# Optimization experiments

Hardware: AMD Instinct MI355X
Metric: run time of the kernel (lower is better)

Reference implementation:

```python
import jax, jax.numpy as jnp
import numpy as np

B, S, D = 4, 2048, 1024
H, Dh = 16, 64


def setup_inputs() -> dict:
    key = jax.random.key(0)
    ks = jax.random.split(key, 9)
    s_in = 1.0 / np.sqrt(D)
    inp = {
        "key": jax.random.normal(ks[0], (B, S, D), jnp.float32),
        "value": jax.random.normal(ks[1], (B, S, D), jnp.float32),
        "query": jax.random.normal(ks[2], (B, S, D), jnp.float32),
        # Linear weights stored as [in, out] (math-equivalent to torch W.T)
        "Wq": jax.random.uniform(ks[3], (D, H * Dh), jnp.float32, -s_in, s_in),
        "bq": jax.random.uniform(ks[4], (H * Dh,), jnp.float32, -s_in, s_in),
        "Wk": jax.random.uniform(ks[5], (D, H * Dh), jnp.float32, -s_in, s_in),
        "bk": jax.random.uniform(ks[6], (H * Dh,), jnp.float32, -s_in, s_in),
        "Wv": jax.random.uniform(ks[7], (D, H * Dh), jnp.float32, -s_in, s_in),
        "bv": jax.random.uniform(ks[8], (H * Dh,), jnp.float32, -s_in, s_in),
    }
    return inp


def reference(key, value, query, Wq, bq, Wk, bk, Wv, bv):
    b, s, _ = key.shape
    # projections -> [B, H, S, Dh]
    q = (query @ Wq + bq).reshape(b, s, H, Dh).transpose(0, 2, 1, 3)
    k = (key @ Wk + bk).reshape(b, s, H, Dh).transpose(0, 2, 1, 3)
    v = (value @ Wv + bv).reshape(b, s, H, Dh).transpose(0, 2, 1, 3)
    scores = jnp.einsum("bhqd,bhkd->bhqk", q, k) / np.sqrt(Dh).astype(np.float32)
    p = jax.nn.softmax(scores, axis=-1)
    out = jnp.einsum("bhqk,bhkd->bhqd", p, v)  # [B, H, S, Dh]
    return out.transpose(0, 2, 1, 3).reshape(b, s, H * Dh)
```

## Files before the change

kernel.cpp:

```cpp
#include <hip/hip_runtime.h>

typedef __bf16 bf16;
typedef __bf16 bf16x8 __attribute__((ext_vector_type(8)));
typedef __bf16 bf16x4 __attribute__((ext_vector_type(4)));
typedef _Float16 f16x2 __attribute__((ext_vector_type(2)));
typedef _Float16 f16x4 __attribute__((ext_vector_type(4)));
typedef _Float16 f16x8 __attribute__((ext_vector_type(8)));
typedef __fp16 h16x2 __attribute__((ext_vector_type(2)));
typedef __fp16 h16x4 __attribute__((ext_vector_type(4)));
typedef float  f32x4  __attribute__((ext_vector_type(4)));
typedef float  f32x16 __attribute__((ext_vector_type(16)));

#define LOG2E 1.44269504088896340736f
#define SCQ (0.125f * LOG2E)

__device__ __forceinline__ void async16(const void* g, void* l) {
  __builtin_amdgcn_global_load_lds(
      (const __attribute__((address_space(1))) unsigned int*)g,
      (__attribute__((address_space(3))) unsigned int*)l, 16, 0, 0);
}

__device__ __forceinline__ f32x4 mfma_bf16(bf16x8 a, bf16x8 b, f32x4 c) {
  return __builtin_amdgcn_mfma_f32_16x16x32_bf16(a, b, c, 0, 0, 0);
}
__device__ __forceinline__ f32x16 mfma32_bf16(bf16x8 a, bf16x8 b, f32x16 c) {
  return __builtin_amdgcn_mfma_f32_32x32x16_bf16(a, b, c, 0, 0, 0);
}
__device__ __forceinline__ f32x16 mfma32x8_f16(f16x4 a, f16x4 b, f32x16 c) {
  return __builtin_amdgcn_mfma_f32_32x32x8f16(a, b, c, 0, 0, 0);
}

__global__ __launch_bounds__(256) void prep(const float* __restrict__ q,
                                            const float* __restrict__ k,
                                            const float* __restrict__ v,
                                            const float* __restrict__ W0,
                                            const float* __restrict__ W1,
                                            const float* __restrict__ W2,
                                            bf16* __restrict__ actb,
                                            bf16* __restrict__ Wt) {
  __shared__ float t[64 * 69];
  const int z = blockIdx.y, tid = threadIdx.x;
  if (blockIdx.x < 4096) {
    const float* in = z == 0 ? q : (z == 1 ? k : v);
    bf16* o = actb + (size_t)z * 8388608;
    int i = blockIdx.x * 256 + tid;
    const float4* p = (const float4*)in;
    float4 a = p[i * 2], c = p[i * 2 + 1];
    bf16x8 r;
    r[0] = (bf16)a.x; r[1] = (bf16)a.y; r[2] = (bf16)a.z; r[3] = (bf16)a.w;
    r[4] = (bf16)c.x; r[5] = (bf16)c.y; r[6] = (bf16)c.z; r[7] = (bf16)c.w;
    ((bf16x8*)o)[i] = r;
  } else {
    const float* W = z == 0 ? W0 : (z == 1 ? W1 : W2);
    bf16* O = Wt + (size_t)z * (1024 * 1024);
    int lin = blockIdx.x - 4096;
    int k0 = (lin & 15) * 64, n0 = (lin >> 4) * 64;
    int r0 = tid >> 4, c0 = (tid & 15) * 4;
#pragma unroll
    for (int rr = 0; rr < 4; rr++) {
      int kk = r0 + rr * 16;
      float4 vv = *(const float4*)(W + (k0 + kk) * 1024 + n0 + c0);
      t[kk * 69 + c0 + 0] = vv.x; t[kk * 69 + c0 + 1] = vv.y;
      t[kk * 69 + c0 + 2] = vv.z; t[kk * 69 + c0 + 3] = vv.w;
    }
    __syncthreads();
#pragma unroll
    for (int rr = 0; rr < 4; rr++) {
      int n = r0 + rr * 16;
      bf16x4 o;
#pragma unroll
      for (int j = 0; j < 4; j++) o[j] = (bf16)t[(c0 + j) * 69 + n];
      *(bf16x4*)(O + (n0 + n) * 1024 + k0 + c0) = o;
    }
  }
}

__global__ __launch_bounds__(256, 3) void gemm_qkv(const bf16* __restrict__ Act,
                                                   const bf16* __restrict__ Wt,
                                                   const float* __restrict__ b0,
                                                   const float* __restrict__ b1,
                                                   const float* __restrict__ b2,
                                                   bf16* __restrict__ qo,
                                                   bf16* __restrict__ ko,
                                                   _Float16* __restrict__ vf) {
  __shared__ bf16 smem[16384];
  bf16* sA = smem;
  bf16* sB = smem + 8192;
  const int tid = threadIdx.x;
  const int wave = tid >> 6, lane = tid & 63;
  const int quad = lane >> 4, l15 = lane & 15;
  const int z = blockIdx.z;
  const int m0 = blockIdx.x * 128, n0 = blockIdx.y * 128;
  const bf16* A = Act + (size_t)z * 8388608;
  const bf16* Bt = Wt + (size_t)z * 1048576;
  const float* bias = z == 0 ? b0 : (z == 1 ? b1 : b2);

  const bf16* ap[4]; const bf16* bp[4]; int lo[4];
#pragma unroll
  for (int i = 0; i < 4; i++) {
    int g = wave * 256 + i * 64 + lane;
    int row = g >> 3, jl = (g & 7) ^ (row & 7);
    ap[i] = A + (m0 + row) * 1024 + jl * 8;
    bp[i] = Bt + (n0 + row) * 1024 + jl * 8;
    lo[i] = (wave * 256 + i * 64) * 8;
  }
  const int wm = (wave & 1) * 64, wn = (wave >> 1) * 64;
  f32x4 acc[4][4] = {};

  for (int kt = 0; kt < 16; kt++) {
    const int ko_ = kt * 64;
#pragma unroll
    for (int i = 0; i < 4; i++) async16(ap[i] + ko_, sA + lo[i]);
#pragma unroll
    for (int i = 0; i < 4; i++) async16(bp[i] + ko_, sB + lo[i]);
    __syncthreads();
#pragma unroll
    for (int ks = 0; ks < 2; ks++) {
      bf16x8 af[4], bv[4];
#pragma unroll
      for (int mt = 0; mt < 4; mt++) {
        int m = wm + mt * 16 + l15;
        int ph = (ks * 4 + quad) ^ (m & 7);
        af[mt] = *(const bf16x8*)(sA + m * 64 + ph * 8);
      }
#pragma unroll
      for (int nt = 0; nt < 4; nt++) {
        int n = wn + nt * 16 + l15;
        int ph = (ks * 4 + quad) ^ (n & 7);
        bv[nt] = *(const bf16x8*)(sB + n * 64 + ph * 8);
      }
#pragma unroll
      for (int mt = 0; mt < 4; mt++)
#pragma unroll
        for (int nt = 0; nt < 4; nt++)
          acc[mt][nt] = mfma_bf16(af[mt], bv[nt], acc[mt][nt]);
    }
    __syncthreads();
  }

  if (z != 2) {
    bf16* O = z == 0 ? qo : ko;
    const float sc = z == 0 ? SCQ : 1.0f;
#pragma unroll
    for (int nt = 0; nt < 4; nt++) {
      int n = n0 + wn + nt * 16 + l15;
      float bc = bias[n];
#pragma unroll
      for (int mt = 0; mt < 4; mt++)
#pragma unroll
        for (int r = 0; r < 4; r++) {
          int m = m0 + wm + mt * 16 + quad * 4 + r;
          O[m * 1024 + n] = (bf16)((acc[mt][nt][r] + bc) * sc);
        }
    }
  } else {
    const int b = m0 >> 11, s0 = m0 & 2047;
    const int kvb = s0 >> 7;
    const int mtg0 = (wave & 1) * 4;
    const int w = quad >> 1, hl = quad & 1;
#pragma unroll
    for (int nt = 0; nt < 4; nt++) {
      int n = n0 + wn + nt * 16;
      int hh = n >> 6, db = (n >> 5) & 1;
      int lanep = hl * 32 + (nt & 1) * 16 + l15;
      float bc = bias[n + l15];
#pragma unroll
      for (int mt = 0; mt < 4; mt++) {
        int fi = (mtg0 + mt) * 2 + db;
        f16x4 pk;
#pragma unroll
        for (int r = 0; r < 4; r++) pk[r] = (_Float16)(acc[mt][nt][r] + bc);
        size_t off = ((((size_t)(b * 16 + hh) * 16 + kvb) * 16 + fi) * 512)
                     + lanep * 8 + w * 4;
        *(f16x4*)(vf + off) = pk;
      }
    }
  }
}

__global__ __launch_bounds__(256, 3) void attn(const bf16* __restrict__ Q,
                                               const bf16* __restrict__ K,
                                               const _Float16* __restrict__ VF,
                                               float* __restrict__ Out) {
  __shared__ bf16 sQ[8192];
  __shared__ bf16 sK[8192];
  __shared__ _Float16 sV[8192];
  const int tid = threadIdx.x;
  const int wave = tid >> 6, lane = tid & 63;
  const int l31 = lane & 31, hl = lane >> 5;
  const int q0 = blockIdx.x * 128, hh = blockIdx.y, b = blockIdx.z;
  const bf16* Kbase = K + (size_t)(b * 2048) * 1024 + hh * 64;
  const _Float16* Vbase = VF + (size_t)(b * 16 + hh) * 131072;

#pragma unroll
  for (int i = 0; i < 4; i++) {
    int g = i * 256 + tid;
    int row = g >> 3, jl = (g & 7) ^ (row & 7);
    async16(Q + (size_t)(b * 2048 + q0 + row) * 1024 + hh * 64 + jl * 8, sQ + g * 8);
    async16(Kbase + (size_t)row * 1024 + jl * 8, sK + g * 8);
    async16(Vbase + g * 8, sV + g * 8);
  }
  __syncthreads();

  bf16x8 qf[4];
  {
    int rowq = wave * 32 + l31, rx = rowq & 7;
#pragma unroll
    for (int i = 0; i < 4; i++)
      qf[i] = *(const bf16x8*)(sQ + rowq * 64 + ((2 * i + hl) ^ rx) * 8);
  }

  f32x16 oacc[2] = {};
  float ls = 0.f;

  for (int kvb = 0; kvb < 16; kvb++) {
#pragma unroll
    for (int t32 = 0; t32 < 4; t32++) {
      int rowk = t32 * 32 + l31, rx = rowk & 7;
      const bf16* kr = sK + rowk * 64;
      f32x16 st = {};
#pragma unroll
      for (int i = 0; i < 4; i++) {
        bf16x8 kf = *(const bf16x8*)(kr + ((2 * i + hl) ^ rx) * 8);
        st = mfma32_bf16(kf, qf[i], st);
      }
      f16x4 pf[4];
      float ps = 0.f;
#pragma unroll
      for (int s = 0; s < 4; s++) {
        float p0 = __builtin_amdgcn_exp2f(st[4 * s + 0]);
        float p1 = __builtin_amdgcn_exp2f(st[4 * s + 1]);
        float p2 = __builtin_amdgcn_exp2f(st[4 * s + 2]);
        float p3 = __builtin_amdgcn_exp2f(st[4 * s + 3]);
        ps += (p0 + p1) + (p2 + p3);
        h16x2 c0 = __builtin_amdgcn_cvt_pkrtz(p0, p1);
        h16x2 c1 = __builtin_amdgcn_cvt_pkrtz(p2, p3);
        h16x4 cc = __builtin_shufflevector(c0, c1, 0, 1, 2, 3);
        pf[s] = __builtin_bit_cast(f16x4, cc);
      }
      ls += ps;
#pragma unroll
      for (int u = 0; u < 2; u++)
#pragma unroll
        for (int db = 0; db < 2; db++) {
          f16x8 va2 = *(const f16x8*)(sV + ((t32 * 4 + u * 2 + db) * 64 + lane) * 8);
          f16x4 vlo = __builtin_shufflevector(va2, va2, 0, 1, 2, 3);
          f16x4 vhi = __builtin_shufflevector(va2, va2, 4, 5, 6, 7);
          oacc[db] = mfma32x8_f16(vlo, pf[2 * u], oacc[db]);
          oacc[db] = mfma32x8_f16(vhi, pf[2 * u + 1], oacc[db]);
        }
    }
    __syncthreads();
    if (kvb < 15) {
      int kn = (kvb + 1) * 128;
#pragma unroll
      for (int i = 0; i < 4; i++) {
        int g = i * 256 + tid;
        int row = g >> 3, jl = (g & 7) ^ (row & 7);
        async16(Kbase + (size_t)(kn + row) * 1024 + jl * 8, sK + g * 8);
        async16(Vbase + (kvb + 1) * 8192 + g * 8, sV + g * 8);
      }
      __syncthreads();
    }
  }

  ls += __shfl_xor(ls, 32);
  float inv = 1.f / ls;
  int qrow = b * 2048 + q0 + wave * 32 + l31;
  float* orow = Out + (size_t)qrow * 1024 + hh * 64;
#pragma unroll
  for (int db = 0; db < 2; db++)
#pragma unroll
    for (int rg = 0; rg < 4; rg++) {
      float4 v;
      v.x = oacc[db][4 * rg + 0] * inv;
      v.y = oacc[db][4 * rg + 1] * inv;
      v.z = oacc[db][4 * rg + 2] * inv;
      v.w = oacc[db][4 * rg + 3] * inv;
      *(float4*)(orow + db * 32 + rg * 8 + 4 * hl) = v;
    }
}

extern "C" void kernel_launch(void* const* d_in, const int* in_sizes, int n_in,
                              void* d_out, int out_size, void* d_ws, size_t ws_size,
                              hipStream_t stream) {
  const float* key   = (const float*)d_in[0];
  const float* value = (const float*)d_in[1];
  const float* query = (const float*)d_in[2];
  const float* Wq = (const float*)d_in[3];
  const float* bq = (const float*)d_in[4];
  const float* Wk = (const float*)d_in[5];
  const float* bk = (const float*)d_in[6];
  const float* Wv = (const float*)d_in[7];
  const float* bv = (const float*)d_in[8];
  float* out = (float*)d_out;

  char* ws = (char*)d_ws;
  bf16* actb   = (bf16*)(ws);
  bf16* wt     = (bf16*)(ws + 50331648);
  bf16* qo     = (bf16*)(ws + 56623104);
  bf16* ko     = (bf16*)(ws + 73400320);
  _Float16* vf = (_Float16*)(ws + 90177536);
  (void)in_sizes; (void)n_in; (void)out_size; (void)ws_size;

  prep<<<dim3(4352, 3), 256, 0, stream>>>(query, key, value, Wq, Wk, Wv, actb, wt);
  gemm_qkv<<<dim3(64, 8, 3), 256, 0, stream>>>(actb, wt, bq, bk, bv, qo, ko, vf);
  attn<<<dim3(16, 16, 4), 256, 0, stream>>>(qo, ko, vf, out);
}
```

Measured before the change: 289.5 us.

## Use 32x32x16 f16 MFMA for PV with permlane32 swap of P fragments

Switches the P·V product from pairs of 32x32x8 f16 MFMAs to single 32x32x16 f16 MFMAs, halving the instruction count for that stage. Because the K=16 operand layout differs, the probability fragments are rearranged across lane halves with permlane32_swap. The V packing written by the projection kernel is changed to match the new operand layout. The swap adds cross-lane permute instructions, and correctness depends on the V layout and the swap agreeing exactly.

```diff
diff --git a/kernel.cpp b/kernel.cpp
--- a/kernel.cpp
+++ b/kernel.cpp
@@ -3,13 +3,13 @@
 typedef __bf16 bf16;
 typedef __bf16 bf16x8 __attribute__((ext_vector_type(8)));
 typedef __bf16 bf16x4 __attribute__((ext_vector_type(4)));
-typedef _Float16 f16x2 __attribute__((ext_vector_type(2)));
 typedef _Float16 f16x4 __attribute__((ext_vector_type(4)));
 typedef _Float16 f16x8 __attribute__((ext_vector_type(8)));
 typedef __fp16 h16x2 __attribute__((ext_vector_type(2)));
-typedef __fp16 h16x4 __attribute__((ext_vector_type(4)));
 typedef float  f32x4  __attribute__((ext_vector_type(4)));
 typedef float  f32x16 __attribute__((ext_vector_type(16)));
+typedef unsigned int uint2v __attribute__((ext_vector_type(2)));
+typedef unsigned int uint4v __attribute__((ext_vector_type(4)));
 
 #define LOG2E 1.44269504088896340736f
 #define SCQ (0.125f * LOG2E)
@@ -26,8 +26,8 @@
 __device__ __forceinline__ f32x16 mfma32_bf16(bf16x8 a, bf16x8 b, f32x16 c) {
   return __builtin_amdgcn_mfma_f32_32x32x16_bf16(a, b, c, 0, 0, 0);
 }
-__device__ __forceinline__ f32x16 mfma32x8_f16(f16x4 a, f16x4 b, f32x16 c) {
-  return __builtin_amdgcn_mfma_f32_32x32x8f16(a, b, c, 0, 0, 0);
+__device__ __forceinline__ f32x16 mfma32x16_f16(f16x8 a, f16x8 b, f32x16 c) {
+  return __builtin_amdgcn_mfma_f32_32x32x16_f16(a, b, c, 0, 0, 0);
 }
 
 __global__ __launch_bounds__(256) void prep(const float* __restrict__ q,
@@ -157,12 +157,12 @@
     const int b = m0 >> 11, s0 = m0 & 2047;
     const int kvb = s0 >> 7;
     const int mtg0 = (wave & 1) * 4;
-    const int w = quad >> 1, hl = quad & 1;
+    const int hl = quad >> 1, jb = (quad & 1) * 4;
 #pragma unroll
     for (int nt = 0; nt < 4; nt++) {
       int n = n0 + wn + nt * 16;
       int hh = n >> 6, db = (n >> 5) & 1;
-      int lanep = hl * 32 + (nt & 1) * 16 + l15;
+      int lanep = hl * 32 + (n & 31) + l15;
       float bc = bias[n + l15];
 #pragma unroll
       for (int mt = 0; mt < 4; mt++) {
@@ -171,7 +171,7 @@
 #pragma unroll
         for (int r = 0; r < 4; r++) pk[r] = (_Float16)(acc[mt][nt][r] + bc);
         size_t off = ((((size_t)(b * 16 + hh) * 16 + kvb) * 16 + fi) * 512)
-                     + lanep * 8 + w * 4;
+                     + lanep * 8 + jb;
         *(f16x4*)(vf + off) = pk;
       }
     }
@@ -224,7 +224,7 @@
         bf16x8 kf = *(const bf16x8*)(kr + ((2 * i + hl) ^ rx) * 8);
         st = mfma32_bf16(kf, qf[i], st);
       }
-      f16x4 pf[4];
+      unsigned int dw[8];
       float ps = 0.f;
 #pragma unroll
       for (int s = 0; s < 4; s++) {
@@ -233,22 +233,27 @@
         float p2 = __builtin_amdgcn_exp2f(st[4 * s + 2]);
         float p3 = __builtin_amdgcn_exp2f(st[4 * s + 3]);
         ps += (p0 + p1) + (p2 + p3);
-        h16x2 c0 = __builtin_amdgcn_cvt_pkrtz(p0, p1);
-        h16x2 c1 = __builtin_amdgcn_cvt_pkrtz(p2, p3);
-        h16x4 cc = __builtin_shufflevector(c0, c1, 0, 1, 2, 3);
-        pf[s] = __builtin_bit_cast(f16x4, cc);
+        dw[2 * s]     = __builtin_bit_cast(unsigned int,
+                          __builtin_amdgcn_cvt_pkrtz(p0, p1));
+        dw[2 * s + 1] = __builtin_bit_cast(unsigned int,
+                          __builtin_amdgcn_cvt_pkrtz(p2, p3));
       }
       ls += ps;
 #pragma unroll
-      for (int u = 0; u < 2; u++)
+      for (int u = 0; u < 2; u++) {
+        uint2v rA = __builtin_amdgcn_permlane32_swap(dw[4 * u + 0],
+                                                     dw[4 * u + 2], false, false);
+        uint2v rB = __builtin_amdgcn_permlane32_swap(dw[4 * u + 1],
+                                                     dw[4 * u + 3], false, false);
+        uint4v uu;
+        uu[0] = rA[0]; uu[1] = rB[0]; uu[2] = rA[1]; uu[3] = rB[1];
+        f16x8 pfrag = __builtin_bit_cast(f16x8, uu);
 #pragma unroll
         for (int db = 0; db < 2; db++) {
-          f16x8 va2 = *(const f16x8*)(sV + ((t32 * 4 + u * 2 + db) * 64 + lane) * 8);
-          f16x4 vlo = __builtin_shufflevector(va2, va2, 0, 1, 2, 3);
-          f16x4 vhi = __builtin_shufflevector(va2, va2, 4, 5, 6, 7);
-          oacc[db] = mfma32x8_f16(vlo, pf[2 * u], oacc[db]);
-          oacc[db] = mfma32x8_f16(vhi, pf[2 * u + 1], oacc[db]);
+          f16x8 va = *(const f16x8*)(sV + ((t32 * 4 + u * 2 + db) * 64 + lane) * 8);
+          oacc[db] = mfma32x16_f16(va, pfrag, oacc[db]);
         }
+      }
     }
     __syncthreads();
     if (kvb < 15) {
```

Measured after the change: 290.8 us. About the same (+0.5%).
